# Kernel optimization log

Hardware: AMD Instinct MI355X
Metric: run time of the kernel (lower is better)

## Reference

```python
import jax, jax.numpy as jnp
import numpy as np


def setup_inputs() -> dict:
    key = jax.random.key(0)
    k1, k2, k3 = jax.random.split(key, 3)
    preds = jax.random.normal(k1, (8, 3, 2048, 8), dtype=jnp.float32)
    gts = jax.random.normal(k2, (8, 3, 2048), dtype=jnp.float32)
    idx = jax.random.randint(k3, (64, 2), 0, 8, dtype=jnp.int64)
    return {"preds": preds, "gts": gts, "idx": idx}


def reference(preds, gts, idx):
    # preds: [bs, 3, N, seeds], gts: [bs, 3, N], idx: [num, 2] (batch, seed)
    num = idx.shape[0]
    # select (batch, seed) pairs -> [num, 3, N]
    p = jnp.transpose(preds, (0, 3, 1, 2))[idx[:, 0], idx[:, 1]]
    # gts expanded over seeds is constant in seed -> just index batch
    g = gts[idx[:, 0]]  # [num, 3, N]
    x = jnp.transpose(p, (0, 2, 1))  # [num, N, 3]
    y = jnp.transpose(g, (0, 2, 1))  # [num, N, 3]
    # P[b, i, j] = ||x_i||^2 + ||y_j||^2 - 2 x_i . y_j
    rx = jnp.sum(x * x, axis=-1)  # [num, N]
    ry = jnp.sum(y * y, axis=-1)  # [num, N]
    zz = jnp.einsum('bid,bjd->bij', x, y)  # [num, N, N]
    P = rx[:, :, None] + ry[:, None, :] - 2.0 * zz
    loss_1 = jnp.sum(jnp.min(P, axis=1))  # min over x for each y
    loss_2 = jnp.sum(jnp.min(P, axis=2))  # min over y for each x
    return (loss_1 + loss_2) / num
```

## Files before the change

kernel.cpp:

```cpp
#include <hip/hip_runtime.h>


#define NPTS 2048
#define NB 64
#define BLK 256

#define PREDS_A 49152
#define PREDS_C 16384
#define GTS_A 6144
#define GTS_C 2048

#define OFF_XMIN  0
#define OFF_YMIN  524288
#define OFF_PART  1048576
#define OFF_XPK   1052672
#define OFF_YPK   5246976
#define WS_REQ    9441280

using bf16x8  = __attribute__((ext_vector_type(8))) __bf16;
using short8v = __attribute__((ext_vector_type(8))) short;
using f32x16  = __attribute__((ext_vector_type(16))) float;

static __device__ __forceinline__ unsigned short f2bf(float f) {
    unsigned u = __float_as_uint(f);
    u = u + 0x7FFFu + ((u >> 16) & 1u);
    return (unsigned short)(u >> 16);
}
static __device__ __forceinline__ float bf2f(unsigned short h) {
    return __uint_as_float(((unsigned)h) << 16);
}
static __device__ __forceinline__ float min3f(float a, float b, float c) {
    return fminf(fminf(a, b), c);
}

__global__ __launch_bounds__(256) void cf_prep3(
    const float* __restrict__ preds, const float* __restrict__ gts,
    const int* __restrict__ idx,
    unsigned short* __restrict__ xpkB, unsigned short* __restrict__ ypkB)
{
    const int blk = blockIdx.x, tid = threadIdx.x;
    const unsigned short one = 0x3F80;
    const int p = (blk & 511) * 256 + tid;
    const int b = p >> 11, j = p & 2047;
    const int i0 = idx[2 * b];
    float v0, v1, v2;
    unsigned short* dstbase;
    if (blk < 512) {
        const int m1 = idx[2 * b + 1];
        const float* pb = preds + i0 * PREDS_A + m1 + j * 8;
        v0 = pb[0]; v1 = pb[PREDS_C]; v2 = pb[2 * PREDS_C];
        dstbase = xpkB;
    } else {
        const float* gb = gts + i0 * GTS_A + j;
        v0 = gb[0]; v1 = gb[GTS_C]; v2 = gb[2 * GTS_C];
        dstbase = ypkB;
    }
    const float rr = fmaf(v0, v0, fmaf(v1, v1, v2 * v2));
    const unsigned short h0 = f2bf(v0), h1 = f2bf(v1), h2 = f2bf(v2);
    const unsigned short l0 = f2bf(v0 - bf2f(h0));
    const unsigned short l1 = f2bf(v1 - bf2f(h1));
    const unsigned short l2 = f2bf(v2 - bf2f(h2));
    const unsigned short rh = f2bf(rr), rl = f2bf(rr - bf2f(rh));
    alignas(16) unsigned short t[16] =
        {h0, h1, h2, l0, l1, l2, h0, h1, h2, one, one, rh, rl, 0, 0, 0};
    uint4* dst = (uint4*)(dstbase + (size_t)p * 16);
    dst[0] = *(const uint4*)&t[0];
    dst[1] = *(const uint4*)&t[8];
}

__global__ __launch_bounds__(BLK, 4) void cf_mf5(
    const float* __restrict__ preds, const float* __restrict__ gts,
    const int* __restrict__ idx,
    const unsigned short* __restrict__ xpkB, const unsigned short* __restrict__ ypkB,
    float* __restrict__ xmin, float* __restrict__ ymin)
{
    const int tid = threadIdx.x;
    const int pass = blockIdx.x >> 10;
    const int strip = blockIdx.x & 15;
    const int b = (blockIdx.x >> 4) & 63;

    const int l = tid & 63, w = tid >> 6;
    const int lc = l & 31, lh = l >> 5;

    const int i0 = idx[2 * b];
    const int row = strip * 128 + w * 32 + lc;
    float x0, x1, x2;
    if (pass == 0) {
        const int m1 = idx[2 * b + 1];
        const float* pb = preds + i0 * PREDS_A + m1 + row * 8;
        x0 = pb[0]; x1 = pb[PREDS_C]; x2 = pb[2 * PREDS_C];
    } else {
        const float* gb = gts + i0 * GTS_A + row;
        x0 = gb[0]; x1 = gb[GTS_C]; x2 = gb[2 * GTS_C];
    }
    const float rx = fmaf(x0, x0, fmaf(x1, x1, x2 * x2));
    const float a0 = -2.f * x0, a1 = -2.f * x1, a2 = -2.f * x2;
    const unsigned short h0 = f2bf(a0), h1 = f2bf(a1), h2 = f2bf(a2);
    const unsigned short lo0 = f2bf(a0 - bf2f(h0));
    const unsigned short lo1 = f2bf(a1 - bf2f(h1));
    const unsigned short lo2 = f2bf(a2 - bf2f(h2));
    const unsigned short rh = f2bf(rx), rl = f2bf(rx - bf2f(rh));
    const unsigned short one = 0x3F80;
    short8v av;
    av[0] = (short)(lh ? lo2 : h0);
    av[1] = (short)(lh ? rh  : h1);
    av[2] = (short)(lh ? rl  : h2);
    av[3] = (short)(lh ? one : h0);
    av[4] = (short)(lh ? one : h1);
    av[5] = (short)(lh ? (unsigned short)0 : h2);
    av[6] = (short)(lh ? (unsigned short)0 : lo0);
    av[7] = (short)(lh ? (unsigned short)0 : lo1);
    const bf16x8 afrag = __builtin_bit_cast(bf16x8, av);

    float rm[16];
#pragma unroll
    for (int r = 0; r < 16; ++r) rm[r] = INFINITY;

    const f32x16 z = {0.f, 0.f, 0.f, 0.f, 0.f, 0.f, 0.f, 0.f,
                      0.f, 0.f, 0.f, 0.f, 0.f, 0.f, 0.f, 0.f};

    const unsigned short* refpk = pass ? xpkB : ypkB;
    const short8v* yp = (const short8v*)refpk + (b * NPTS * 2 + lc * 2 + lh);

    bf16x8 curA = __builtin_bit_cast(bf16x8, yp[0]);
    bf16x8 curB = __builtin_bit_cast(bf16x8, yp[64]);

#pragma unroll 2
    for (int s = 0; s < 32; ++s) {
        const int nidx = (s < 31) ? (2 * s + 2) * 64 : 0;
        const bf16x8 nxtA = __builtin_bit_cast(bf16x8, yp[nidx]);
        const bf16x8 nxtB = __builtin_bit_cast(bf16x8, yp[nidx + 64]);

        __builtin_amdgcn_s_setprio(1);
        f32x16 accA = __builtin_amdgcn_mfma_f32_32x32x16_bf16(afrag, curA, z, 0, 0, 0);
        f32x16 accB = __builtin_amdgcn_mfma_f32_32x32x16_bf16(afrag, curB, z, 0, 0, 0);
        __builtin_amdgcn_s_setprio(0);

#pragma unroll
        for (int r = 0; r < 16; ++r) rm[r] = min3f(accA[r], accB[r], rm[r]);

        curA = nxtA; curB = nxtB;
    }

#pragma unroll
    for (int r = 0; r < 16; ++r) {
        float v = rm[r];
        v = fminf(v, __shfl_xor(v, 1, 32));
        v = fminf(v, __shfl_xor(v, 2, 32));
        v = fminf(v, __shfl_xor(v, 4, 32));
        v = fminf(v, __shfl_xor(v, 8, 32));
        v = fminf(v, __shfl_xor(v, 16, 32));
        rm[r] = v;
    }
    if (lc == 0) {
        float* outbuf = pass ? ymin : xmin;
        const int rbase = b * NPTS + strip * 128 + w * 32 + 4 * lh;
#pragma unroll
        for (int r = 0; r < 16; ++r)
            outbuf[rbase + (r & 3) + 8 * (r >> 2)] = fmaxf(rm[r], 0.f);
    }
}

__global__ __launch_bounds__(256) void cf_red1(
    const float* __restrict__ xmin, const float* __restrict__ ymin,
    float* __restrict__ partial)
{
    __shared__ float sm[4];
    const int blk = blockIdx.x, tid = threadIdx.x;
    const float* rp = (blk < 64) ? (xmin + blk * 2048) : (ymin + (blk - 64) * 2048);
    float s = 0.0f;
#pragma unroll
    for (int i = 0; i < 8; ++i) s += rp[tid + i * 256];
#pragma unroll
    for (int off = 32; off > 0; off >>= 1)
        s += __shfl_down(s, off, 64);
    if ((tid & 63) == 0) sm[tid >> 6] = s;
    __syncthreads();
    if (tid == 0) partial[blk] = sm[0] + sm[1] + sm[2] + sm[3];
}

__global__ __launch_bounds__(256) void cf_red2(const float* __restrict__ partial,
                                               float* __restrict__ out) {
    __shared__ float sm[4];
    float s = (threadIdx.x < 128) ? partial[threadIdx.x] : 0.f;
#pragma unroll
    for (int off = 32; off > 0; off >>= 1)
        s += __shfl_down(s, off, 64);
    if ((threadIdx.x & 63) == 0) sm[threadIdx.x >> 6] = s;
    __syncthreads();
    if (threadIdx.x == 0)
        out[0] = (sm[0] + sm[1] + sm[2] + sm[3]) * (1.0f / 64.0f);
}

#define NMIN (2 * NB * NPTS)
#define FIT 128
#define FJT 128
#define PADI(j) ((j) + ((j) >> 4))

__global__ __launch_bounds__(256) void cf_init(unsigned* __restrict__ colbuf) {
    int i = blockIdx.x * 256 + threadIdx.x;
    colbuf[i] = 0x7F800000u;
}

__global__ __launch_bounds__(BLK, 4) void cf_tile_lds(
    const float* __restrict__ preds, const float* __restrict__ gts,
    const int* __restrict__ idx, unsigned* __restrict__ minbuf)
{
    const int tid = threadIdx.x;
    const int bid = blockIdx.x;
    const int it = bid & 15;
    const int b = bid >> 4;
    const int i0 = idx[2 * b];
    const int m1 = idx[2 * b + 1];
    const float* pbase = preds + i0 * PREDS_A + m1;
    const float* gbase = gts + i0 * GTS_A;

    __shared__ float4 sq[PADI(FIT - 1) + 2];
    __shared__ float4 sr[PADI(NPTS - 1) + 2];
    __shared__ float  scolw[4][FJT];

    if (tid < FIT) {
        const int i = it * FIT + tid;
        const float q0 = pbase[i * 8];
        const float q1 = pbase[i * 8 + PREDS_C];
        const float q2 = pbase[i * 8 + 2 * PREDS_C];
        const float rq = fmaf(q0, q0, fmaf(q1, q1, q2 * q2));
        sq[PADI(tid)] = make_float4(-2.f * q0, -2.f * q1, -2.f * q2, rq);
    }
#pragma unroll
    for (int k = 0; k < 8; ++k) {
        const int j = tid + BLK * k;
        const float r0 = gbase[j];
        const float r1 = gbase[j + GTS_C];
        const float r2 = gbase[j + 2 * GTS_C];
        const float rr = fmaf(r0, r0, fmaf(r1, r1, r2 * r2));
        sr[PADI(j)] = make_float4(r0, r1, r2, rr);
    }
    __syncthreads();

    const int ty = tid >> 4, tx = tid & 15;
    float nq0[8], nq1[8], nq2[8], rq[8], rmin[8];
#pragma unroll
    for (int u = 0; u < 8; ++u) {
        const float4 q = sq[PADI(ty * 8 + u)];
        nq0[u] = q.x; nq1[u] = q.y; nq2[u] = q.z; rq[u] = q.w;
        rmin[u] = INFINITY;
    }
    unsigned* rowbuf = minbuf;
    unsigned* colbuf = minbuf + NB * NPTS;

    for (int jt = 0; jt < NPTS / FJT; ++jt) {
        float4 r[8];
        const int rb = PADI(jt * FJT + tx * 8);
#pragma unroll
        for (int v = 0; v < 8; ++v) r[v] = sr[rb + v];
        float cmin[8];
#pragma unroll
        for (int v = 0; v < 8; ++v) cmin[v] = INFINITY;
#pragma unroll
        for (int v = 0; v < 8; v += 2) {
#pragma unroll
            for (int u = 0; u < 8; u += 2) {
                float s00 = fmaf(nq2[u], r[v].z, r[v].w);
                s00 = fmaf(nq1[u], r[v].y, s00);
                s00 = fmaf(nq0[u], r[v].x, s00);
                float s01 = fmaf(nq2[u], r[v + 1].z, r[v + 1].w);
                s01 = fmaf(nq1[u], r[v + 1].y, s01);
                s01 = fmaf(nq0[u], r[v + 1].x, s01);
                float s10 = fmaf(nq2[u + 1], r[v].z, r[v].w);
                s10 = fmaf(nq1[u + 1], r[v].y, s10);
                s10 = fmaf(nq0[u + 1], r[v].x, s10);
                float s11 = fmaf(nq2[u + 1], r[v + 1].z, r[v + 1].w);
                s11 = fmaf(nq1[u + 1], r[v + 1].y, s11);
                s11 = fmaf(nq0[u + 1], r[v + 1].x, s11);
                rmin[u]     = min3f(s00, s01, rmin[u]);
                rmin[u + 1] = min3f(s10, s11, rmin[u + 1]);
                const float d00 = s00 + rq[u];
                const float d10 = s10 + rq[u + 1];
                const float d01 = s01 + rq[u];
                const float d11 = s11 + rq[u + 1];
                cmin[v]     = min3f(d00, d10, cmin[v]);
                cmin[v + 1] = min3f(d01, d11, cmin[v + 1]);
            }
        }
#pragma unroll
        for (int v = 0; v < 8; ++v) {
            float c = cmin[v];
            c = fminf(c, __shfl_xor(c, 16, 64));
            c = fminf(c, __shfl_xor(c, 32, 64));
            cmin[v] = c;
        }
        if (((tid >> 4) & 3) == 0) {
            const int w = tid >> 6;
            *(float4*)&scolw[w][tx * 8]     = make_float4(cmin[0], cmin[1], cmin[2], cmin[3]);
            *(float4*)&scolw[w][tx * 8 + 4] = make_float4(cmin[4], cmin[5], cmin[6], cmin[7]);
        }
        __syncthreads();
        if (tid < FJT) {
            float m = fminf(min3f(scolw[0][tid], scolw[1][tid], scolw[2][tid]), scolw[3][tid]);
            m = fmaxf(m, 0.0f);
            atomicMin(&colbuf[b * NPTS + jt * FJT + tid], __float_as_uint(m));
        }
        __syncthreads();
    }
#pragma unroll
    for (int u = 0; u < 8; ++u) {
        float rm = rmin[u];
        rm = fminf(rm, __shfl_xor(rm, 1, 16));
        rm = fminf(rm, __shfl_xor(rm, 2, 16));
        rm = fminf(rm, __shfl_xor(rm, 4, 16));
        rm = fminf(rm, __shfl_xor(rm, 8, 16));
        rmin[u] = rm;
    }
    if (tx == 0) {
#pragma unroll
        for (int u = 0; u < 8; ++u) {
            const float d = fmaxf(rmin[u] + rq[u], 0.0f);
            rowbuf[b * NPTS + it * FIT + ty * 8 + u] = __float_as_uint(d);
        }
    }
}

__global__ __launch_bounds__(256) void cf_reduce1(const unsigned* __restrict__ minbuf,
                                                  float* __restrict__ partial) {
    __shared__ float sm[4];
    const int base = blockIdx.x * 1024;
    float s = 0.0f;
    for (int k = threadIdx.x; k < 1024; k += 256)
        s += __uint_as_float(minbuf[base + k]);
#pragma unroll
    for (int off = 32; off > 0; off >>= 1)
        s += __shfl_down(s, off, 64);
    if ((threadIdx.x & 63) == 0) sm[threadIdx.x >> 6] = s;
    __syncthreads();
    if (threadIdx.x == 0)
        partial[blockIdx.x] = sm[0] + sm[1] + sm[2] + sm[3];
}

__global__ __launch_bounds__(256) void cf_reduce2(const float* __restrict__ partial,
                                                  float* __restrict__ out) {
    __shared__ float sm[4];
    float s = (threadIdx.x < 128) ? partial[threadIdx.x] : 0.f;
#pragma unroll
    for (int off = 32; off > 0; off >>= 1)
        s += __shfl_down(s, off, 64);
    if ((threadIdx.x & 63) == 0) sm[threadIdx.x >> 6] = s;
    __syncthreads();
    if (threadIdx.x == 0)
        out[0] = (sm[0] + sm[1] + sm[2] + sm[3]) * (1.0f / 64.0f);
}

extern "C" void kernel_launch(void* const* d_in, const int* in_sizes, int n_in,
                              void* d_out, int out_size, void* d_ws, size_t ws_size,
                              hipStream_t stream) {
    const float* preds = (const float*)d_in[0];
    const float* gts   = (const float*)d_in[1];
    const int*   idx   = (const int*)d_in[2];
    float* out = (float*)d_out;

    if (ws_size >= (size_t)WS_REQ) {
        float* xmin = (float*)((char*)d_ws + OFF_XMIN);
        float* ymin = (float*)((char*)d_ws + OFF_YMIN);
        float* partial = (float*)((char*)d_ws + OFF_PART);
        unsigned short* xpkB = (unsigned short*)((char*)d_ws + OFF_XPK);
        unsigned short* ypkB = (unsigned short*)((char*)d_ws + OFF_YPK);
        cf_prep3<<<1024, 256, 0, stream>>>(preds, gts, idx, xpkB, ypkB);
        cf_mf5<<<2 * NB * 16, BLK, 0, stream>>>(preds, gts, idx, xpkB, ypkB, xmin, ymin);
        cf_red1<<<128, 256, 0, stream>>>(xmin, ymin, partial);
        cf_red2<<<1, 256, 0, stream>>>(partial, out);
    } else {
        unsigned* minbuf = (unsigned*)d_ws;
        unsigned* colbuf = minbuf + NB * NPTS;
        float* partial   = (float*)((char*)d_ws + NMIN * 4);
        cf_init<<<(NB * NPTS) / 256, 256, 0, stream>>>(colbuf);
        cf_tile_lds<<<NB * (NPTS / FIT), BLK, 0, stream>>>(preds, gts, idx, minbuf);
        cf_reduce1<<<NMIN / 1024, 256, 0, stream>>>(minbuf, partial);
        cf_reduce2<<<1, 256, 0, stream>>>(partial, out);
    }
}
```

Before: 41.31 us.

## Register-block two row tiles per wave and fuse row-min sum into MFMA kernel

Each wave now builds two A fragments covering 64 rows and reuses every loaded reference fragment for four MFMAs instead of two. This halves reference-point loads per MFMA and halves the grid. The per-row minima are clamped and summed inside the MFMA kernel and written as one partial per block. That removes the xmin/ymin buffers and the intermediate reduction launch, and the final reduction now sums 1024 partials. The cost is higher register use (two min arrays, four accumulators) and fewer blocks to hide latency.

```diff
diff --git a/kernel.cpp b/kernel.cpp
--- a/kernel.cpp
+++ b/kernel.cpp
@@ -10,12 +10,10 @@
 #define GTS_A 6144
 #define GTS_C 2048
 
-#define OFF_XMIN  0
-#define OFF_YMIN  524288
-#define OFF_PART  1048576
-#define OFF_XPK   1052672
-#define OFF_YPK   5246976
-#define WS_REQ    9441280
+#define OFF_PART  0
+#define OFF_XPK   4096
+#define OFF_YPK   4198400
+#define WS_REQ    8392704
 
 using bf16x8  = __attribute__((ext_vector_type(8))) __bf16;
 using short8v = __attribute__((ext_vector_type(8))) short;
@@ -31,6 +29,27 @@
 }
 static __device__ __forceinline__ float min3f(float a, float b, float c) {
     return fminf(fminf(a, b), c);
+}
+
+static __device__ __forceinline__ bf16x8 makeA(float x0, float x1, float x2, int lh) {
+    const float rx = fmaf(x0, x0, fmaf(x1, x1, x2 * x2));
+    const float a0 = -2.f * x0, a1 = -2.f * x1, a2 = -2.f * x2;
+    const unsigned short h0 = f2bf(a0), h1 = f2bf(a1), h2 = f2bf(a2);
+    const unsigned short lo0 = f2bf(a0 - bf2f(h0));
+    const unsigned short lo1 = f2bf(a1 - bf2f(h1));
+    const unsigned short lo2 = f2bf(a2 - bf2f(h2));
+    const unsigned short rh = f2bf(rx), rl = f2bf(rx - bf2f(rh));
+    const unsigned short one = 0x3F80;
+    short8v av;
+    av[0] = (short)(lh ? lo2 : h0);
+    av[1] = (short)(lh ? rh  : h1);
+    av[2] = (short)(lh ? rl  : h2);
+    av[3] = (short)(lh ? one : h0);
+    av[4] = (short)(lh ? one : h1);
+    av[5] = (short)(lh ? (unsigned short)0 : h2);
+    av[6] = (short)(lh ? (unsigned short)0 : lo0);
+    av[7] = (short)(lh ? (unsigned short)0 : lo1);
+    return __builtin_bit_cast(bf16x8, av);
 }
 
 __global__ __launch_bounds__(256) void cf_prep3(
@@ -68,53 +87,42 @@
     dst[1] = *(const uint4*)&t[8];
 }
 
-__global__ __launch_bounds__(BLK, 4) void cf_mf5(
+__global__ __launch_bounds__(BLK, 4) void cf_mf6(
     const float* __restrict__ preds, const float* __restrict__ gts,
     const int* __restrict__ idx,
     const unsigned short* __restrict__ xpkB, const unsigned short* __restrict__ ypkB,
-    float* __restrict__ xmin, float* __restrict__ ymin)
+    float* __restrict__ partial)
 {
     const int tid = threadIdx.x;
-    const int pass = blockIdx.x >> 10;
-    const int strip = blockIdx.x & 15;
-    const int b = (blockIdx.x >> 4) & 63;
+    const int bid = blockIdx.x;
+    const int pass = bid >> 9;
+    const int b = (bid >> 3) & 63;
+    const int strip = bid & 7;
+
+    __shared__ float smw[4];
 
     const int l = tid & 63, w = tid >> 6;
     const int lc = l & 31, lh = l >> 5;
 
     const int i0 = idx[2 * b];
-    const int row = strip * 128 + w * 32 + lc;
-    float x0, x1, x2;
+    const int row0 = strip * 256 + w * 64 + lc;
+    float x0a, x1a, x2a, x0b, x1b, x2b;
     if (pass == 0) {
         const int m1 = idx[2 * b + 1];
-        const float* pb = preds + i0 * PREDS_A + m1 + row * 8;
-        x0 = pb[0]; x1 = pb[PREDS_C]; x2 = pb[2 * PREDS_C];
+        const float* pb = preds + i0 * PREDS_A + m1 + row0 * 8;
+        x0a = pb[0];   x1a = pb[PREDS_C];       x2a = pb[2 * PREDS_C];
+        x0b = pb[256]; x1b = pb[PREDS_C + 256]; x2b = pb[2 * PREDS_C + 256];
     } else {
-        const float* gb = gts + i0 * GTS_A + row;
-        x0 = gb[0]; x1 = gb[GTS_C]; x2 = gb[2 * GTS_C];
-    }
-    const float rx = fmaf(x0, x0, fmaf(x1, x1, x2 * x2));
-    const float a0 = -2.f * x0, a1 = -2.f * x1, a2 = -2.f * x2;
-    const unsigned short h0 = f2bf(a0), h1 = f2bf(a1), h2 = f2bf(a2);
-    const unsigned short lo0 = f2bf(a0 - bf2f(h0));
-    const unsigned short lo1 = f2bf(a1 - bf2f(h1));
-    const unsigned short lo2 = f2bf(a2 - bf2f(h2));
-    const unsigned short rh = f2bf(rx), rl = f2bf(rx - bf2f(rh));
-    const unsigned short one = 0x3F80;
-    short8v av;
-    av[0] = (short)(lh ? lo2 : h0);
-    av[1] = (short)(lh ? rh  : h1);
-    av[2] = (short)(lh ? rl  : h2);
-    av[3] = (short)(lh ? one : h0);
-    av[4] = (short)(lh ? one : h1);
-    av[5] = (short)(lh ? (unsigned short)0 : h2);
-    av[6] = (short)(lh ? (unsigned short)0 : lo0);
-    av[7] = (short)(lh ? (unsigned short)0 : lo1);
-    const bf16x8 afrag = __builtin_bit_cast(bf16x8, av);
-
-    float rm[16];
-#pragma unroll
-    for (int r = 0; r < 16; ++r) rm[r] = INFINITY;
+        const float* gb = gts + i0 * GTS_A + row0;
+        x0a = gb[0];  x1a = gb[GTS_C];      x2a = gb[2 * GTS_C];
+        x0b = gb[32]; x1b = gb[GTS_C + 32]; x2b = gb[2 * GTS_C + 32];
+    }
+    const bf16x8 af0 = makeA(x0a, x1a, x2a, lh);
+    const bf16x8 af1 = makeA(x0b, x1b, x2b, lh);
+
+    float rmA[16], rmB[16];
+#pragma unroll
+    for (int r = 0; r < 16; ++r) { rmA[r] = INFINITY; rmB[r] = INFINITY; }
 
     const f32x16 z = {0.f, 0.f, 0.f, 0.f, 0.f, 0.f, 0.f, 0.f,
                       0.f, 0.f, 0.f, 0.f, 0.f, 0.f, 0.f, 0.f};
@@ -132,57 +140,52 @@
         const bf16x8 nxtB = __builtin_bit_cast(bf16x8, yp[nidx + 64]);
 
         __builtin_amdgcn_s_setprio(1);
-        f32x16 accA = __builtin_amdgcn_mfma_f32_32x32x16_bf16(afrag, curA, z, 0, 0, 0);
-        f32x16 accB = __builtin_amdgcn_mfma_f32_32x32x16_bf16(afrag, curB, z, 0, 0, 0);
+        f32x16 acc0A = __builtin_amdgcn_mfma_f32_32x32x16_bf16(af0, curA, z, 0, 0, 0);
+        f32x16 acc0B = __builtin_amdgcn_mfma_f32_32x32x16_bf16(af0, curB, z, 0, 0, 0);
         __builtin_amdgcn_s_setprio(0);
-
-#pragma unroll
-        for (int r = 0; r < 16; ++r) rm[r] = min3f(accA[r], accB[r], rm[r]);
+#pragma unroll
+        for (int r = 0; r < 16; ++r) rmA[r] = min3f(acc0A[r], acc0B[r], rmA[r]);
+
+        __builtin_amdgcn_s_setprio(1);
+        f32x16 acc1A = __builtin_amdgcn_mfma_f32_32x32x16_bf16(af1, curA, z, 0, 0, 0);
+        f32x16 acc1B = __builtin_amdgcn_mfma_f32_32x32x16_bf16(af1, curB, z, 0, 0, 0);
+        __builtin_amdgcn_s_setprio(0);
+#pragma unroll
+        for (int r = 0; r < 16; ++r) rmB[r] = min3f(acc1A[r], acc1B[r], rmB[r]);
 
         curA = nxtA; curB = nxtB;
     }
 
+    float lsum = 0.f;
 #pragma unroll
     for (int r = 0; r < 16; ++r) {
-        float v = rm[r];
-        v = fminf(v, __shfl_xor(v, 1, 32));
-        v = fminf(v, __shfl_xor(v, 2, 32));
-        v = fminf(v, __shfl_xor(v, 4, 32));
-        v = fminf(v, __shfl_xor(v, 8, 32));
-        v = fminf(v, __shfl_xor(v, 16, 32));
-        rm[r] = v;
-    }
-    if (lc == 0) {
-        float* outbuf = pass ? ymin : xmin;
-        const int rbase = b * NPTS + strip * 128 + w * 32 + 4 * lh;
-#pragma unroll
-        for (int r = 0; r < 16; ++r)
-            outbuf[rbase + (r & 3) + 8 * (r >> 2)] = fmaxf(rm[r], 0.f);
-    }
-}
-
-__global__ __launch_bounds__(256) void cf_red1(
-    const float* __restrict__ xmin, const float* __restrict__ ymin,
-    float* __restrict__ partial)
-{
+        float va = rmA[r], vb = rmB[r];
+        va = fminf(va, __shfl_xor(va, 1, 32));
+        va = fminf(va, __shfl_xor(va, 2, 32));
+        va = fminf(va, __shfl_xor(va, 4, 32));
+        va = fminf(va, __shfl_xor(va, 8, 32));
+        va = fminf(va, __shfl_xor(va, 16, 32));
+        vb = fminf(vb, __shfl_xor(vb, 1, 32));
+        vb = fminf(vb, __shfl_xor(vb, 2, 32));
+        vb = fminf(vb, __shfl_xor(vb, 4, 32));
+        vb = fminf(vb, __shfl_xor(vb, 8, 32));
+        vb = fminf(vb, __shfl_xor(vb, 16, 32));
+        lsum += fmaxf(va, 0.f) + fmaxf(vb, 0.f);
+    }
+    lsum = (lc == 0) ? lsum : 0.f;
+    lsum += __shfl_xor(lsum, 32, 64);
+    if (l == 0) smw[w] = lsum;
+    __syncthreads();
+    if (tid == 0)
+        partial[bid] = smw[0] + smw[1] + smw[2] + smw[3];
+}
+
+__global__ __launch_bounds__(256) void cf_red2b(const float* __restrict__ partial,
+                                                float* __restrict__ out) {
     __shared__ float sm[4];
-    const int blk = blockIdx.x, tid = threadIdx.x;
-    const float* rp = (blk < 64) ? (xmin + blk * 2048) : (ymin + (blk - 64) * 2048);
-    float s = 0.0f;
-#pragma unroll
-    for (int i = 0; i < 8; ++i) s += rp[tid + i * 256];
-#pragma unroll
-    for (int off = 32; off > 0; off >>= 1)
-        s += __shfl_down(s, off, 64);
-    if ((tid & 63) == 0) sm[tid >> 6] = s;
-    __syncthreads();
-    if (tid == 0) partial[blk] = sm[0] + sm[1] + sm[2] + sm[3];
-}
-
-__global__ __launch_bounds__(256) void cf_red2(const float* __restrict__ partial,
-                                               float* __restrict__ out) {
-    __shared__ float sm[4];
-    float s = (threadIdx.x < 128) ? partial[threadIdx.x] : 0.f;
+    float s = 0.f;
+#pragma unroll
+    for (int i = 0; i < 4; ++i) s += partial[threadIdx.x + i * 256];
 #pragma unroll
     for (int off = 32; off > 0; off >>= 1)
         s += __shfl_down(s, off, 64);
@@ -359,15 +362,12 @@
     float* out = (float*)d_out;
 
     if (ws_size >= (size_t)WS_REQ) {
-        float* xmin = (float*)((char*)d_ws + OFF_XMIN);
-        float* ymin = (float*)((char*)d_ws + OFF_YMIN);
         float* partial = (float*)((char*)d_ws + OFF_PART);
         unsigned short* xpkB = (unsigned short*)((char*)d_ws + OFF_XPK);
         unsigned short* ypkB = (unsigned short*)((char*)d_ws + OFF_YPK);
         cf_prep3<<<1024, 256, 0, stream>>>(preds, gts, idx, xpkB, ypkB);
-        cf_mf5<<<2 * NB * 16, BLK, 0, stream>>>(preds, gts, idx, xpkB, ypkB, xmin, ymin);
-        cf_red1<<<128, 256, 0, stream>>>(xmin, ymin, partial);
-        cf_red2<<<1, 256, 0, stream>>>(partial, out);
+        cf_mf6<<<2 * NB * 8, BLK, 0, stream>>>(preds, gts, idx, xpkB, ypkB, partial);
+        cf_red2b<<<1, 256, 0, stream>>>(partial, out);
     } else {
         unsigned* minbuf = (unsigned*)d_ws;
         unsigned* colbuf = minbuf + NB * NPTS;
```

After: 38.47 us. 6.9% less time.
